# Optimization experiments

Measured on AMD Instinct MI355X. Metric: run time of the kernel, lower is better.

The kernel has to match this reference:

```python
import jax, jax.numpy as jnp
import numpy as np


def _bidir_linear_rnn(x, kernel, rec):
    """Bidirectional SimpleRNN(units=1, activation=None, use_bias=False).
    x: [B, T, 1]; kernel, rec: [1, 1]. Returns [B, T, 2] (concat fw/bw).
    Linear recurrence h_t = k*x_t + r*h_{t-1} computed as an associative scan.
    """
    k = kernel[0, 0]
    r = rec[0, 0]

    def scan_dir(xs):
        u = xs * k                       # [B, T, 1]
        a = jnp.full_like(u, r)          # decay per step (constant)

        def combine(c1, c2):
            a1, b1 = c1
            a2, b2 = c2
            return (a1 * a2, a2 * b1 + b2)

        _, h = jax.lax.associative_scan(combine, (a, u), axis=1)
        return h                         # [B, T, 1]

    fw = scan_dir(x)
    bw = jnp.flip(scan_dir(jnp.flip(x, axis=1)), axis=1)
    return jnp.concatenate([fw, bw], axis=-1)  # [B, T, 2]


def setup_inputs() -> dict:
    key = jax.random.key(0)
    B, T, D = 4096, 4096, 1
    x = jax.random.normal(key, (B, T, D), dtype=jnp.float32)
    kernel = jnp.ones((1, 1), dtype=jnp.float32)           # toy_kernel = 1.0
    rec = -0.5 * jnp.ones((1, 1), dtype=jnp.float32)       # toy_recurrent_kernel = -0.5
    return {"x": x, "kernel": kernel, "rec": rec}


def reference(x, kernel, rec):
    out_stateless = _bidir_linear_rnn(x, kernel, rec)
    # Stateful layer has identical weights and zero initial states on first call,
    # so its output equals the stateless output; diff is their difference.
    out_stateful = _bidir_linear_rnn(x, kernel, rec)
    diff = out_stateful - out_stateless
    return (out_stateless, diff)
```

## Files before the change

kernel.cpp:

```cpp
#include <hip/hip_runtime.h>


constexpr int T_LEN  = 4096;
constexpr int SEG    = 16;
constexpr int NT     = 256;
constexpr int NW     = NT / 64;
constexpr int ROW_F4 = T_LEN * 2 / 4;
constexpr int LDS_F4 = (ROW_F4 / 8) * 9;

__global__ __launch_bounds__(NT) void bidir_rnn(
    const float* __restrict__ x,
    const float* __restrict__ kp,
    const float* __restrict__ rp,
    float*       __restrict__ out,
    float*       __restrict__ diff)
{
    const int b    = blockIdx.x;
    const int tid  = threadIdx.x;
    const int lane = tid & 63;
    const int wv   = tid >> 6;
    const float k = *kp;
    const float r = *rp;

    float pw[SEG + 1];
    pw[0] = 1.0f;
    #pragma unroll
    for (int i = 1; i <= SEG; ++i) pw[i] = pw[i - 1] * r;
    const float a16 = pw[SEG];

    const size_t rowbase = (size_t)b * T_LEN;

    const float4* xin = (const float4*)(x + rowbase) + tid * 4;
    float4 v0 = xin[0], v1 = xin[1], v2 = xin[2], v3 = xin[3];
    float u[SEG] = {v0.x, v0.y, v0.z, v0.w, v1.x, v1.y, v1.z, v1.w,
                    v2.x, v2.y, v2.z, v2.w, v3.x, v3.y, v3.z, v3.w};
    #pragma unroll
    for (int j = 0; j < SEG; ++j) u[j] *= k;

    float lf[SEG], lb[SEG];
    lf[0] = u[0];
    #pragma unroll
    for (int j = 1; j < SEG; ++j) lf[j] = fmaf(r, lf[j - 1], u[j]);
    lb[SEG - 1] = u[SEG - 1];
    #pragma unroll
    for (int j = SEG - 2; j >= 0; --j) lb[j] = fmaf(r, lb[j + 1], u[j]);

    float af = a16, bf = lf[SEG - 1];
    #pragma unroll
    for (int off = 1; off < 64; off <<= 1) {
        float ap = __shfl_up(af, off);
        float bp = __shfl_up(bf, off);
        if (lane >= off) { bf = fmaf(af, bp, bf); af *= ap; }
    }
    float aef = __shfl_up(af, 1), bef = __shfl_up(bf, 1);
    if (lane == 0) { aef = 1.0f; bef = 0.0f; }

    float ab = a16, bb = lb[0];
    #pragma unroll
    for (int off = 1; off < 64; off <<= 1) {
        float ap = __shfl_down(ab, off);
        float bp = __shfl_down(bb, off);
        if (lane < 64 - off) { bb = fmaf(ab, bp, bb); ab *= ap; }
    }
    float aeb = __shfl_down(ab, 1), beb = __shfl_down(bb, 1);
    if (lane == 63) { aeb = 1.0f; beb = 0.0f; }

    __shared__ float4 sOut[LDS_F4];
    __shared__ float sWa[NW], sWb[NW], sVa[NW], sVb[NW];
    if (lane == 63) { sWa[wv] = af; sWb[wv] = bf; }
    if (lane == 0)  { sVa[wv] = ab; sVb[wv] = bb; }
    __syncthreads();

    float Pb = 0.0f;
    #pragma unroll
    for (int w = 0; w < NW - 1; ++w) {
        if (w < wv) { Pb = fmaf(sWa[w], Pb, sWb[w]); }
    }
    const float Hf = fmaf(aef, Pb, bef);

    float Qb = 0.0f;
    #pragma unroll
    for (int w = NW - 1; w > 0; --w) {
        if (w > wv) { Qb = fmaf(sVa[w], Qb, sVb[w]); }
    }
    const float Hb = fmaf(aeb, Qb, beb);

    #pragma unroll
    for (int q = 0; q < 8; ++q) {
        const int j0 = 2 * q, j1 = 2 * q + 1;
        float4 o;
        o.x = fmaf(pw[j0 + 1],   Hf, lf[j0]);
        o.y = fmaf(pw[SEG - j0], Hb, lb[j0]);
        o.z = fmaf(pw[j1 + 1],   Hf, lf[j1]);
        o.w = fmaf(pw[SEG - j1], Hb, lb[j1]);
        sOut[tid * 9 + q] = o;
    }
    __syncthreads();

    float4* orow = (float4*)(out + rowbase * 2);
    #pragma unroll
    for (int q2 = 0; q2 < 8; ++q2) {
        const int f4 = q2 * NT + tid;
        orow[f4] = sOut[(f4 >> 3) * 9 + (f4 & 7)];
    }

    float4* d = (float4*)(diff + rowbase * 2) + tid;
    const float4 z = make_float4(0.0f, 0.0f, 0.0f, 0.0f);
    #pragma unroll
    for (int m = 0; m < 8; ++m) d[m * NT] = z;
}

extern "C" void kernel_launch(void* const* d_in, const int* in_sizes, int n_in,
                              void* d_out, int out_size, void* d_ws, size_t ws_size,
                              hipStream_t stream) {
    const float* x  = (const float*)d_in[0];
    const float* kp = (const float*)d_in[1];
    const float* rp = (const float*)d_in[2];
    float* out = (float*)d_out;

    const int B = in_sizes[0] / T_LEN;
    float* diff = out + (size_t)B * T_LEN * 2;

    bidir_rnn<<<dim3(B), dim3(NT), 0, stream>>>(x, kp, rp, out, diff);
}
```

Baseline: 319.0 us.

## Write outputs directly from registers and zero diff with memset

Removes the LDS staging buffer and its barrier, so each thread writes its 8 float4 outputs directly to global memory as contiguous 128-byte chunks. The diff tensor is now zeroed by a separate hipMemsetAsync instead of in-kernel stores, and the backward local scan reuses the u array in place to save registers. Direct stores are less coalesced per instruction (each lane has a 128B stride), and the memset adds a second launch.

Result: no change. 315.5 us (-1.1%).

```diff
diff --git a/kernel.cpp b/kernel.cpp
--- a/kernel.cpp
+++ b/kernel.cpp
@@ -1,19 +1,16 @@
 #include <hip/hip_runtime.h>
 
 
-constexpr int T_LEN  = 4096;
-constexpr int SEG    = 16;
-constexpr int NT     = 256;
-constexpr int NW     = NT / 64;
-constexpr int ROW_F4 = T_LEN * 2 / 4;
-constexpr int LDS_F4 = (ROW_F4 / 8) * 9;
+constexpr int T_LEN = 4096;
+constexpr int SEG   = 16;
+constexpr int NT    = 256;
+constexpr int NW    = NT / 64;
 
 __global__ __launch_bounds__(NT) void bidir_rnn(
     const float* __restrict__ x,
     const float* __restrict__ kp,
     const float* __restrict__ rp,
-    float*       __restrict__ out,
-    float*       __restrict__ diff)
+    float*       __restrict__ out)
 {
     const int b    = blockIdx.x;
     const int tid  = threadIdx.x;
@@ -37,13 +34,12 @@
     #pragma unroll
     for (int j = 0; j < SEG; ++j) u[j] *= k;
 
-    float lf[SEG], lb[SEG];
+    float lf[SEG];
     lf[0] = u[0];
     #pragma unroll
     for (int j = 1; j < SEG; ++j) lf[j] = fmaf(r, lf[j - 1], u[j]);
-    lb[SEG - 1] = u[SEG - 1];
     #pragma unroll
-    for (int j = SEG - 2; j >= 0; --j) lb[j] = fmaf(r, lb[j + 1], u[j]);
+    for (int j = SEG - 2; j >= 0; --j) u[j] = fmaf(r, u[j + 1], u[j]);
 
     float af = a16, bf = lf[SEG - 1];
     #pragma unroll
@@ -55,7 +51,7 @@
     float aef = __shfl_up(af, 1), bef = __shfl_up(bf, 1);
     if (lane == 0) { aef = 1.0f; bef = 0.0f; }
 
-    float ab = a16, bb = lb[0];
+    float ab = a16, bb = u[0];
     #pragma unroll
     for (int off = 1; off < 64; off <<= 1) {
         float ap = __shfl_down(ab, off);
@@ -65,7 +61,6 @@
     float aeb = __shfl_down(ab, 1), beb = __shfl_down(bb, 1);
     if (lane == 63) { aeb = 1.0f; beb = 0.0f; }
 
-    __shared__ float4 sOut[LDS_F4];
     __shared__ float sWa[NW], sWb[NW], sVa[NW], sVb[NW];
     if (lane == 63) { sWa[wv] = af; sWb[wv] = bf; }
     if (lane == 0)  { sVa[wv] = ab; sVb[wv] = bb; }
@@ -85,29 +80,17 @@
     }
     const float Hb = fmaf(aeb, Qb, beb);
 
+    float4* o = (float4*)(out + rowbase * 2) + tid * 8;
     #pragma unroll
-    for (int q = 0; q < 8; ++q) {
-        const int j0 = 2 * q, j1 = 2 * q + 1;
-        float4 o;
-        o.x = fmaf(pw[j0 + 1],   Hf, lf[j0]);
-        o.y = fmaf(pw[SEG - j0], Hb, lb[j0]);
-        o.z = fmaf(pw[j1 + 1],   Hf, lf[j1]);
-        o.w = fmaf(pw[SEG - j1], Hb, lb[j1]);
-        sOut[tid * 9 + q] = o;
+    for (int m = 0; m < 8; ++m) {
+        const int j0 = 2 * m, j1 = 2 * m + 1;
+        float4 v;
+        v.x = fmaf(pw[j0 + 1],   Hf, lf[j0]);
+        v.y = fmaf(pw[SEG - j0], Hb, u[j0]);
+        v.z = fmaf(pw[j1 + 1],   Hf, lf[j1]);
+        v.w = fmaf(pw[SEG - j1], Hb, u[j1]);
+        o[m] = v;
     }
-    __syncthreads();
-
-    float4* orow = (float4*)(out + rowbase * 2);
-    #pragma unroll
-    for (int q2 = 0; q2 < 8; ++q2) {
-        const int f4 = q2 * NT + tid;
-        orow[f4] = sOut[(f4 >> 3) * 9 + (f4 & 7)];
-    }
-
-    float4* d = (float4*)(diff + rowbase * 2) + tid;
-    const float4 z = make_float4(0.0f, 0.0f, 0.0f, 0.0f);
-    #pragma unroll
-    for (int m = 0; m < 8; ++m) d[m * NT] = z;
 }
 
 extern "C" void kernel_launch(void* const* d_in, const int* in_sizes, int n_in,
@@ -121,5 +104,7 @@
     const int B = in_sizes[0] / T_LEN;
     float* diff = out + (size_t)B * T_LEN * 2;
 
-    bidir_rnn<<<dim3(B), dim3(NT), 0, stream>>>(x, kp, rp, out, diff);
+    hipMemsetAsync(diff, 0, (size_t)B * T_LEN * 2 * sizeof(float), stream);
+
+    bidir_rnn<<<dim3(B), dim3(NT), 0, stream>>>(x, kp, rp, out);
 }
```
